# Kernel tuning notes

Hardware: AMD Instinct MI355X
Metric: run time of the kernel (lower is better)

Reference implementation:

```python
import jax, jax.numpy as jnp
import numpy as np

B, N, D, R, STEPS = 16, 512, 512, 8, 2


def setup_inputs() -> dict:
    key = jax.random.key(0)
    ks = jax.random.split(key, 8)
    nodes = jax.random.normal(ks[0], (B, N, D), dtype=jnp.float32)
    edges = jax.random.uniform(ks[1], (B, R, N, N), dtype=jnp.float32)
    scale = 1.0 / np.sqrt(D)
    # per-relation Linear layers: weight [out,in] torch-style, bias [out]
    msg_W = jax.random.uniform(ks[2], (R, D, D), minval=-scale, maxval=scale, dtype=jnp.float32)
    msg_b = jax.random.uniform(ks[3], (R, D), minval=-scale, maxval=scale, dtype=jnp.float32)
    # GRUCell params, gate order (r, z, n) like torch
    w_ih = jax.random.uniform(ks[4], (3 * D, D), minval=-scale, maxval=scale, dtype=jnp.float32)
    w_hh = jax.random.uniform(ks[5], (3 * D, D), minval=-scale, maxval=scale, dtype=jnp.float32)
    b_ih = jax.random.uniform(ks[6], (3 * D,), minval=-scale, maxval=scale, dtype=jnp.float32)
    b_hh = jax.random.uniform(ks[7], (3 * D,), minval=-scale, maxval=scale, dtype=jnp.float32)
    return {"nodes": nodes, "edges": edges, "msg_W": msg_W, "msg_b": msg_b,
            "w_ih": w_ih, "w_hh": w_hh, "b_ih": b_ih, "b_hh": b_hh}


def reference(nodes, edges, msg_W, msg_b, w_ih, w_hh, b_ih, b_hh):
    # nodes: [b,n,d], edges: [b,R,n,n]
    h = nodes  # keep [b,n,d]; torch flattens to [b*n,d] but math is identical
    bias_sum = msg_b.sum(axis=0)  # sum of per-relation biases, [d]
    for _ in range(STEPS):
        # per-relation message passing: m[b,r,i,d] = edges[b,r] @ h[b]
        m = jnp.einsum('brij,bjd->brid', edges, h)
        # per-relation Linear (y = x @ W_r^T + b_r), summed over relations
        agg = jnp.einsum('brid,red->bie', m, msg_W) + bias_sum  # [b,n,d]
        # GRUCell update (gate order r, z, n)
        gi = agg @ w_ih.T + b_ih  # [b,n,3d]
        gh = h @ w_hh.T + b_hh    # [b,n,3d]
        ir, iz, i_n = jnp.split(gi, 3, axis=-1)
        hr, hz, h_n = jnp.split(gh, 3, axis=-1)
        r = jax.nn.sigmoid(ir + hr)
        z = jax.nn.sigmoid(iz + hz)
        n_t = jnp.tanh(i_n + r * h_n)
        h = (1.0 - z) * n_t + z * h
    return h.mean(axis=1)  # [b,d]
```

## Files before the change

### kernel.cpp

```cpp
#include <hip/hip_runtime.h>

typedef _Float16 f16;
typedef __attribute__((ext_vector_type(8))) _Float16 half8;
typedef __attribute__((ext_vector_type(4))) float f32x4;

struct f16x4 { f16 a, b, c, d; };


__device__ __forceinline__ void stage16(const f16* g, f16* l) {
  __builtin_amdgcn_global_load_lds(
      (const __attribute__((address_space(1))) void*)g,
      (__attribute__((address_space(3))) void*)l, 16, 0, 0);
}

__global__ void cvt_fr(const float* __restrict__ in, f16* __restrict__ hi,
                       f16* __restrict__ lo, int n_units) {
  const int u = blockIdx.x * blockDim.x + threadIdx.x;
  if (u >= n_units) return;
  const int l = u & 63, kc = (u >> 6) & 15, rt = u >> 10;
  const long ibase = (long)(rt * 16 + (l & 15)) * 512 + kc * 32 + ((l >> 4) << 3);
  const float4 v0 = *(const float4*)(in + ibase);
  const float4 v1 = *(const float4*)(in + ibase + 4);
  const float v[8] = {v0.x, v0.y, v0.z, v0.w, v1.x, v1.y, v1.z, v1.w};
  half8 h, lw;
#pragma unroll
  for (int e = 0; e < 8; ++e) {
    h[e] = (f16)v[e];
    lw[e] = (f16)(v[e] - (float)h[e]);
  }
  *(half8*)(hi + (long)u * 8) = h;
  *(half8*)(lo + (long)u * 8) = lw;
}

__global__ void cvt_fr1(const float* __restrict__ in, f16* __restrict__ hi,
                        int n_units) {
  const int u = blockIdx.x * blockDim.x + threadIdx.x;
  if (u >= n_units) return;
  const int l = u & 63, kc = (u >> 6) & 15, rt = u >> 10;
  const long ibase = (long)(rt * 16 + (l & 15)) * 512 + kc * 32 + ((l >> 4) << 3);
  const float4 v0 = *(const float4*)(in + ibase);
  const float4 v1 = *(const float4*)(in + ibase + 4);
  const float v[8] = {v0.x, v0.y, v0.z, v0.w, v1.x, v1.y, v1.z, v1.w};
  half8 h;
#pragma unroll
  for (int e = 0; e < 8; ++e) h[e] = (f16)v[e];
  *(half8*)(hi + (long)u * 8) = h;
}

__global__ void bias_sum_k(const float* __restrict__ msg_b, float* __restrict__ bs) {
  int e = threadIdx.x;
  float s = 0.f;
  for (int r = 0; r < 8; ++r) s += msg_b[r * 512 + e];
  bs[e] = s;
}

template <int SA, int SB, int OUT, int SWZ>
__global__ __launch_bounds__(256, 3) void gemm_dr(
    const f16* __restrict__ Ah, const f16* __restrict__ Al,
    const f16* __restrict__ Bh, const f16* __restrict__ Bl,
    f16* __restrict__ Chi, f16* __restrict__ Clo, float* __restrict__ Cf,
    const float* __restrict__ bias, int N, int R, long sAr, long sBr,
    int zdiv, long sAzr, long sAzb, long sBzr, long sBzb,
    long sCzr, long sCzb) {
  constexpr int NU = 8 * ((1 + SA) + (1 + SB));
  constexpr int NW = NU / 4;
  constexpr int BUF = NU * 512;
  constexpr int SMEMN = (2 * BUF > 16384) ? 2 * BUF : 16384;
  __shared__ __align__(16) f16 smem[SMEMN];

  const int tid = threadIdx.x;
  int bx, by, z;
  if constexpr (SWZ) {
    const int l = blockIdx.x;
    const int xcd = l & 7, m2 = l >> 3, zq = m2 >> 4, t = m2 & 15;
    z = (zq << 3) | xcd; bx = t & 3; by = t >> 2;
  } else {
    bx = blockIdx.x; by = blockIdx.y; z = blockIdx.z;
  }
  const int zr = z % zdiv, zb = z / zdiv;
  const int lane = tid & 63;
  const int w = tid >> 6;
  const int wm = (w & 1) << 6;
  const int wn = (w >> 1) << 6;

  const f16* gA = Ah + (long)zr * sAzr + (long)zb * sAzb + (long)by * 65536 + lane * 8;
  const f16* gB = Bh + (long)zr * sBzr + (long)zb * sBzb + (long)bx * 65536 + lane * 8;
  const f16* gAl = SA ? (Al + (gA - Ah)) : nullptr;
  const f16* gBl = SB ? (Bl + (gB - Bh)) : nullptr;
  const long cbase = (long)zr * sCzr + (long)zb * sCzb;

  f32x4 acc[4][4];
#pragma unroll
  for (int i = 0; i < 4; ++i)
#pragma unroll
    for (int j = 0; j < 4; ++j) acc[i][j] = (f32x4){0.f, 0.f, 0.f, 0.f};

  const int NIT = R * 16;

  auto ST = [&](int bf, int ii) {
    const long oa = (long)(ii >> 4) * sAr + (ii & 15) * 512;
    const long ob = (long)(ii >> 4) * sBr + (ii & 15) * 512;
    f16* lb = &smem[bf * BUF];
#pragma unroll
    for (int q = 0; q < NW; ++q) {
      const int s = w * NW + q;
      const f16* src;
      if (s < 8) {
        src = gA + (long)s * 8192 + oa;
      } else if (SA && s < 16) {
        src = gAl + (long)(s - 8) * 8192 + oa;
      } else {
        const int sb = s - 8 * (1 + SA);
        src = (SB && sb >= 8) ? (gBl + (long)(sb - 8) * 8192 + ob)
                              : (gB + (long)sb * 8192 + ob);
      }
      stage16(src, lb + s * 512);
    }
  };

  auto CP = [&](int bf) {
    const f16* lb = &smem[bf * BUF];
    const int lo8 = lane * 8;
    half8 bh[4], bl[4];
#pragma unroll
    for (int nt = 0; nt < 4; ++nt) {
      const int ub = 8 * (1 + SA) + (w >> 1) * 4 + nt;
      bh[nt] = *(const half8*)(lb + ub * 512 + lo8);
      if constexpr (SB) bl[nt] = *(const half8*)(lb + (ub + 8) * 512 + lo8);
    }
#pragma unroll
    for (int mt = 0; mt < 4; ++mt) {
      const int ua = (w & 1) * 4 + mt;
      const half8 ah = *(const half8*)(lb + ua * 512 + lo8);
      half8 al;
      if constexpr (SA) al = *(const half8*)(lb + (ua + 8) * 512 + lo8);
#pragma unroll
      for (int nt = 0; nt < 4; ++nt) {
        acc[mt][nt] = __builtin_amdgcn_mfma_f32_16x16x32_f16(
            ah, bh[nt], acc[mt][nt], 0, 0, 0);
        if constexpr (SB)
          acc[mt][nt] = __builtin_amdgcn_mfma_f32_16x16x32_f16(
              ah, bl[nt], acc[mt][nt], 0, 0, 0);
        if constexpr (SA)
          acc[mt][nt] = __builtin_amdgcn_mfma_f32_16x16x32_f16(
              al, bh[nt], acc[mt][nt], 0, 0, 0);
      }
    }
  };

  auto WAITN = [&]() {
    if constexpr (NW == 4)      asm volatile("s_waitcnt vmcnt(4)" ::: "memory");
    else if constexpr (NW == 6) asm volatile("s_waitcnt vmcnt(6)" ::: "memory");
    else if constexpr (NW == 8) asm volatile("s_waitcnt vmcnt(8)" ::: "memory");
    else                        asm volatile("s_waitcnt vmcnt(0)" ::: "memory");
  };

  ST(0, 0);
  ST(1, 1);
  int cur = 0;
  for (int t = 0; t < NIT; ++t) {
    if (t < NIT - 1) WAITN();
    else asm volatile("s_waitcnt vmcnt(0)" ::: "memory");
    __builtin_amdgcn_s_barrier();
    __builtin_amdgcn_sched_barrier(0);
    CP(cur);
    asm volatile("s_waitcnt lgkmcnt(0)" ::: "memory");
    __builtin_amdgcn_s_barrier();
    if (t + 2 < NIT) ST(cur, t + 2);
    cur ^= 1;
  }
  __syncthreads();

  const int l15 = lane & 15;
  const int rb = (lane >> 4) << 2;
  if constexpr (OUT) {
#pragma unroll
    for (int nt = 0; nt < 4; ++nt) {
      const int col = wn + nt * 16 + l15;
#pragma unroll
      for (int mt = 0; mt < 4; ++mt)
#pragma unroll
        for (int v = 0; v < 4; ++v) {
          const int row = wm + mt * 16 + rb + v;
          const float cval = acc[mt][nt][v];
          const f16 h = (f16)cval;
          smem[row * 128 + ((col >> 3) ^ (row & 15)) * 8 + (col & 7)] = h;
          acc[mt][nt][v] = cval - (float)h;
        }
    }
    __syncthreads();
#pragma unroll
    for (int i2 = 0; i2 < 8; ++i2) {
      const int u = i2 * 256 + tid;
      const int ul = u & 63, kc_loc = (u >> 6) & 3, rt_loc = u >> 8;
      const int row = rt_loc * 16 + (ul & 15);
      const int gcol = kc_loc * 4 + (ul >> 4);
      const int4 vv = *(const int4*)&smem[row * 128 + ((gcol ^ (row & 15)) << 3)];
      *(int4*)&Chi[cbase + ((long)(by * 8 + rt_loc) * 16 + bx * 4 + kc_loc) * 512 + ul * 8] = vv;
    }
    __syncthreads();
#pragma unroll
    for (int nt = 0; nt < 4; ++nt) {
      const int col = wn + nt * 16 + l15;
#pragma unroll
      for (int mt = 0; mt < 4; ++mt)
#pragma unroll
        for (int v = 0; v < 4; ++v) {
          const int row = wm + mt * 16 + rb + v;
          smem[row * 128 + ((col >> 3) ^ (row & 15)) * 8 + (col & 7)] = (f16)acc[mt][nt][v];
        }
    }
    __syncthreads();
#pragma unroll
    for (int i2 = 0; i2 < 8; ++i2) {
      const int u = i2 * 256 + tid;
      const int ul = u & 63, kc_loc = (u >> 6) & 3, rt_loc = u >> 8;
      const int row = rt_loc * 16 + (ul & 15);
      const int gcol = kc_loc * 4 + (ul >> 4);
      const int4 vv = *(const int4*)&smem[row * 128 + ((gcol ^ (row & 15)) << 3)];
      *(int4*)&Clo[cbase + ((long)(by * 8 + rt_loc) * 16 + bx * 4 + kc_loc) * 512 + ul * 8] = vv;
    }
  } else {
#pragma unroll
    for (int nt = 0; nt < 4; ++nt) {
      const int col = bx * 128 + wn + nt * 16 + l15;
      const float bv = bias ? bias[col] : 0.f;
#pragma unroll
      for (int mt = 0; mt < 4; ++mt) {
        const long rowbase = (long)(by * 128 + wm + mt * 16 + rb) * N + col;
#pragma unroll
        for (int v = 0; v < 4; ++v)
          Cf[cbase + rowbase + (long)v * N] = acc[mt][nt][v] + bv;
      }
    }
  }
}

__global__ void reduce_agg2(const f16* __restrict__ Phi, const f16* __restrict__ Plo,
                            const float* __restrict__ bsum,
                            f16* __restrict__ hi, f16* __restrict__ lo) {
  const long i = ((long)blockIdx.x * blockDim.x + threadIdx.x) * 4;
  const int li = (int)i;
  const int l = (li >> 3) & 63, kc = (li >> 9) & 15;
  const int e0 = kc * 32 + ((l >> 4) << 3) + (li & 4);
  const float4 b = *(const float4*)(bsum + e0);
  float v0 = b.x, v1 = b.y, v2 = b.z, v3 = b.w;
#pragma unroll
  for (int q = 0; q < 2; ++q) {
    const long o = (long)q * 4194304 + i;
    const f16x4 ph = *(const f16x4*)(Phi + o);
    const f16x4 pl = *(const f16x4*)(Plo + o);
    v0 += (float)ph.a + (float)pl.a;
    v1 += (float)ph.b + (float)pl.b;
    v2 += (float)ph.c + (float)pl.c;
    v3 += (float)ph.d + (float)pl.d;
  }
  f16x4 h, lw;
  h.a = (f16)v0; lw.a = (f16)(v0 - (float)h.a);
  h.b = (f16)v1; lw.b = (f16)(v1 - (float)h.b);
  h.c = (f16)v2; lw.c = (f16)(v2 - (float)h.c);
  h.d = (f16)v3; lw.d = (f16)(v3 - (float)h.d);
  *(f16x4*)(hi + i) = h;
  *(f16x4*)(lo + i) = lw;
}

__global__ void gru_k(const float* __restrict__ gi, const float* __restrict__ gh,
                      const float* __restrict__ holdf, f16* __restrict__ hhi) {
  const int u = blockIdx.x * blockDim.x + threadIdx.x;
  const int row = u >> 6, d0 = (u & 63) << 3;
  const long gbase = (long)row * 1536 + d0;
  const float4 giR0 = *(const float4*)(gi + gbase),      giR1 = *(const float4*)(gi + gbase + 4);
  const float4 giZ0 = *(const float4*)(gi + gbase + 512), giZ1 = *(const float4*)(gi + gbase + 516);
  const float4 giN0 = *(const float4*)(gi + gbase + 1024), giN1 = *(const float4*)(gi + gbase + 1028);
  const float4 ghR0 = *(const float4*)(gh + gbase),      ghR1 = *(const float4*)(gh + gbase + 4);
  const float4 ghZ0 = *(const float4*)(gh + gbase + 512), ghZ1 = *(const float4*)(gh + gbase + 516);
  const float4 ghN0 = *(const float4*)(gh + gbase + 1024), ghN1 = *(const float4*)(gh + gbase + 1028);
  const float irv[8] = {giR0.x, giR0.y, giR0.z, giR0.w, giR1.x, giR1.y, giR1.z, giR1.w};
  const float izv[8] = {giZ0.x, giZ0.y, giZ0.z, giZ0.w, giZ1.x, giZ1.y, giZ1.z, giZ1.w};
  const float inv[8] = {giN0.x, giN0.y, giN0.z, giN0.w, giN1.x, giN1.y, giN1.z, giN1.w};
  const float hrv[8] = {ghR0.x, ghR0.y, ghR0.z, ghR0.w, ghR1.x, ghR1.y, ghR1.z, ghR1.w};
  const float hzv[8] = {ghZ0.x, ghZ0.y, ghZ0.z, ghZ0.w, ghZ1.x, ghZ1.y, ghZ1.z, ghZ1.w};
  const float hnv[8] = {ghN0.x, ghN0.y, ghN0.z, ghN0.w, ghN1.x, ghN1.y, ghN1.z, ghN1.w};
  const long hflat = (long)(row >> 4) * 8192 + (d0 >> 5) * 512 +
                     ((row & 15) + (((d0 >> 3) & 3) << 4)) * 8;
  half8 hh8;
  if (!holdf) hh8 = *(const half8*)(hhi + hflat);
  half8 oh;
#pragma unroll
  for (int e = 0; e < 8; ++e) {
    const float h = holdf ? holdf[(long)row * 512 + d0 + e] : (float)hh8[e];
    const float r = 1.f / (1.f + __expf(-(irv[e] + hrv[e])));
    const float zg = 1.f / (1.f + __expf(-(izv[e] + hzv[e])));
    const float nt = tanhf(inv[e] + r * hnv[e]);
    const float o = (1.f - zg) * nt + zg * h;
    oh[e] = (f16)o;
  }
  *(half8*)(hhi + hflat) = oh;
}

__global__ void mean_k(const f16* __restrict__ hhi, float* __restrict__ out) {
  const int b = blockIdx.x;
  const int d = threadIdx.x;
  const long base = (long)b * 262144 + (d >> 5) * 512 + (((d >> 3) & 3) << 4) * 8 + (d & 7);
  float s = 0.f;
  for (int n = 0; n < 512; ++n) {
    const long j = base + (long)(n >> 4) * 8192 + (n & 15) * 8;
    s += (float)hhi[j];
  }
  out[b * 512 + d] = s * (1.f / 512.f);
}

extern "C" void kernel_launch(void* const* d_in, const int* in_sizes, int n_in,
                              void* d_out, int out_size, void* d_ws, size_t ws_size,
                              hipStream_t stream) {
  const float* nodes = (const float*)d_in[0];
  const float* edges = (const float*)d_in[1];
  const float* msg_W = (const float*)d_in[2];
  const float* msg_b = (const float*)d_in[3];
  const float* w_ih  = (const float*)d_in[4];
  const float* w_hh  = (const float*)d_in[5];
  const float* b_ih  = (const float*)d_in[6];
  const float* b_hh  = (const float*)d_in[7];
  float* out = (float*)d_out;

  char* ws = (char*)d_ws;
  size_t off = 0;
  auto alloc = [&](size_t bytes) -> char* {
    char* p = ws + off;
    off += (bytes + 1023) & ~(size_t)1023;
    return p;
  };
  f16* edges_hi = (f16*)alloc(33554432ull * 2);
  f16* W_hi     = (f16*)alloc(2097152ull * 2);
  f16* W_lo     = (f16*)alloc(2097152ull * 2);
  f16* wih_hi   = (f16*)alloc(786432ull * 2);
  f16* whh_hi   = (f16*)alloc(786432ull * 2);
  f16* h_hi     = (f16*)alloc(4194304ull * 2);
  f16* hWT_hi   = (f16*)alloc(33554432ull * 2);
  f16* hWT_lo   = (f16*)alloc(33554432ull * 2);
  f16* Phi      = (f16*)alloc(16777216ull * 2);
  f16* Plo      = (f16*)alloc(16777216ull * 2);
  float* bsum   = (float*)alloc(512 * 4);
  float* gi = (float*)hWT_hi;
  float* gh = (float*)hWT_lo;
  f16* agg_hi = hWT_hi + 25165824;
  f16* agg_lo = agg_hi + 4194304;

  cvt_fr1<<<16384, 256, 0, stream>>>(edges, edges_hi, 4194304);
  cvt_fr<<<1024,  256, 0, stream>>>(msg_W, W_hi, W_lo, 262144);
  cvt_fr1<<<384,  256, 0, stream>>>(w_ih, wih_hi, 98304);
  cvt_fr1<<<384,  256, 0, stream>>>(w_hh, whh_hi, 98304);
  cvt_fr1<<<2048, 256, 0, stream>>>(nodes, h_hi, 524288);
  bias_sum_k<<<1, 512, 0, stream>>>(msg_b, bsum);

  for (int step = 0; step < 2; ++step) {
    gemm_dr<1, 0, 1, 0><<<dim3(4, 4, 128), 256, 0, stream>>>(
        W_hi, W_lo, h_hi, nullptr, hWT_hi, hWT_lo, nullptr, nullptr,
        512, 1, 0L, 0L, 8, 262144L, 0L, 0L, 262144L, 262144L, 2097152L);
    gemm_dr<0, 1, 1, 1><<<dim3(512, 1, 1), 256, 0, stream>>>(
        edges_hi, nullptr, hWT_hi, hWT_lo, Phi, Plo, nullptr, nullptr,
        512, 4, 262144L, 262144L, 2, 1048576L, 2097152L, 1048576L, 2097152L,
        4194304L, 262144L);
    reduce_agg2<<<4096, 256, 0, stream>>>(Phi, Plo, bsum, agg_hi, agg_lo);
    gemm_dr<1, 0, 0, 0><<<dim3(12, 64, 1), 256, 0, stream>>>(
        agg_hi, agg_lo, wih_hi, nullptr, nullptr, nullptr, gi, b_ih,
        1536, 1, 0L, 0L, 1, 0L, 0L, 0L, 0L, 0L, 0L);
    gemm_dr<0, 0, 0, 0><<<dim3(12, 64, 1), 256, 0, stream>>>(
        h_hi, nullptr, whh_hi, nullptr, nullptr, nullptr, gh, b_hh,
        1536, 1, 0L, 0L, 1, 0L, 0L, 0L, 0L, 0L, 0L);
    gru_k<<<2048, 256, 0, stream>>>(gi, gh, step ? nullptr : nodes, h_hi);
  }
  mean_k<<<16, 512, 0, stream>>>(h_hi, out);
}
```

Measured before the change: 727.3 us.

## Fuse GRU input/hidden GEMMs into one launch, split mean reduction, merge weight conversions

The two GRU projection GEMMs (agg·W_ih and h·W_hh) now run as a single launch, with block x-index selecting which one a block computes, through a dedicated double-buffered LDS-staged MFMA body. The final mean is split into a two-stage reduction over 256 blocks instead of 16, and the two weight conversions are merged into one launch. gru_k now always reads h from the f16 buffer instead of the fp32 nodes on the first step. That drops some precision on the first step's old-h term, and the new GEMM path hardcodes dimensions.

```diff
diff --git a/kernel.cpp b/kernel.cpp
--- a/kernel.cpp
+++ b/kernel.cpp
@@ -36,6 +36,24 @@
                         int n_units) {
   const int u = blockIdx.x * blockDim.x + threadIdx.x;
   if (u >= n_units) return;
+  const int l = u & 63, kc = (u >> 6) & 15, rt = u >> 10;
+  const long ibase = (long)(rt * 16 + (l & 15)) * 512 + kc * 32 + ((l >> 4) << 3);
+  const float4 v0 = *(const float4*)(in + ibase);
+  const float4 v1 = *(const float4*)(in + ibase + 4);
+  const float v[8] = {v0.x, v0.y, v0.z, v0.w, v1.x, v1.y, v1.z, v1.w};
+  half8 h;
+#pragma unroll
+  for (int e = 0; e < 8; ++e) h[e] = (f16)v[e];
+  *(half8*)(hi + (long)u * 8) = h;
+}
+
+__global__ void cvt_fr1_2(const float* __restrict__ inA, f16* __restrict__ hiA,
+                          const float* __restrict__ inB, f16* __restrict__ hiB,
+                          int nA) {
+  int u = blockIdx.x * blockDim.x + threadIdx.x;
+  const float* in = inA;
+  f16* hi = hiA;
+  if (u >= nA) { u -= nA; in = inB; hi = hiB; }
   const int l = u & 63, kc = (u >> 6) & 15, rt = u >> 10;
   const long ibase = (long)(rt * 16 + (l & 15)) * 512 + kc * 32 + ((l >> 4) << 3);
   const float4 v0 = *(const float4*)(in + ibase);
@@ -236,6 +254,112 @@
   }
 }
 
+template <int SA>
+__device__ __forceinline__ void gemm_body(
+    const f16* __restrict__ Ah, const f16* __restrict__ Al,
+    const f16* __restrict__ Bh, float* __restrict__ Cf,
+    const float* __restrict__ bias, int bx, int by, f16* smem) {
+  constexpr int NU = 8 * (1 + SA) + 8;
+  constexpr int NW = NU / 4;
+  constexpr int BUF = NU * 512;
+
+  const int tid = threadIdx.x;
+  const int lane = tid & 63;
+  const int w = tid >> 6;
+  const int wm = (w & 1) << 6;
+  const int wn = (w >> 1) << 6;
+
+  const f16* gA = Ah + (long)by * 65536 + lane * 8;
+  const f16* gB = Bh + (long)bx * 65536 + lane * 8;
+  const f16* gAl = SA ? (Al + (gA - Ah)) : nullptr;
+
+  f32x4 acc[4][4];
+#pragma unroll
+  for (int i = 0; i < 4; ++i)
+#pragma unroll
+    for (int j = 0; j < 4; ++j) acc[i][j] = (f32x4){0.f, 0.f, 0.f, 0.f};
+
+  auto ST = [&](int bf, int ii) {
+    const long oa = (long)ii * 512;
+    f16* lb = &smem[bf * BUF];
+#pragma unroll
+    for (int q = 0; q < NW; ++q) {
+      const int s = w * NW + q;
+      const f16* src;
+      if (s < 8) src = gA + (long)s * 8192 + oa;
+      else if (SA && s < 16) src = gAl + (long)(s - 8) * 8192 + oa;
+      else src = gB + (long)(s - 8 * (1 + SA)) * 8192 + oa;
+      stage16(src, lb + s * 512);
+    }
+  };
+  auto CP = [&](int bf) {
+    const f16* lb = &smem[bf * BUF];
+    const int lo8 = lane * 8;
+    half8 bh[4];
+#pragma unroll
+    for (int nt = 0; nt < 4; ++nt)
+      bh[nt] = *(const half8*)(lb + (8 * (1 + SA) + (w >> 1) * 4 + nt) * 512 + lo8);
+#pragma unroll
+    for (int mt = 0; mt < 4; ++mt) {
+      const int ua = (w & 1) * 4 + mt;
+      const half8 ah = *(const half8*)(lb + ua * 512 + lo8);
+      half8 al;
+      if constexpr (SA) al = *(const half8*)(lb + (ua + 8) * 512 + lo8);
+#pragma unroll
+      for (int nt = 0; nt < 4; ++nt) {
+        acc[mt][nt] = __builtin_amdgcn_mfma_f32_16x16x32_f16(ah, bh[nt], acc[mt][nt], 0, 0, 0);
+        if constexpr (SA)
+          acc[mt][nt] = __builtin_amdgcn_mfma_f32_16x16x32_f16(al, bh[nt], acc[mt][nt], 0, 0, 0);
+      }
+    }
+  };
+  auto WAITN = [&]() {
+    if constexpr (NW == 4) asm volatile("s_waitcnt vmcnt(4)" ::: "memory");
+    else                   asm volatile("s_waitcnt vmcnt(6)" ::: "memory");
+  };
+
+  ST(0, 0);
+  ST(1, 1);
+  int cur = 0;
+  for (int t = 0; t < 16; ++t) {
+    if (t < 15) WAITN();
+    else asm volatile("s_waitcnt vmcnt(0)" ::: "memory");
+    __builtin_amdgcn_s_barrier();
+    __builtin_amdgcn_sched_barrier(0);
+    CP(cur);
+    asm volatile("s_waitcnt lgkmcnt(0)" ::: "memory");
+    __builtin_amdgcn_s_barrier();
+    if (t + 2 < 16) ST(cur, t + 2);
+    cur ^= 1;
+  }
+
+  const int l15 = lane & 15;
+  const int rb = (lane >> 4) << 2;
+#pragma unroll
+  for (int nt = 0; nt < 4; ++nt) {
+    const int col = bx * 128 + wn + nt * 16 + l15;
+    const float bv = bias[col];
+#pragma unroll
+    for (int mt = 0; mt < 4; ++mt) {
+      const long rowbase = (long)(by * 128 + wm + mt * 16 + rb) * 1536 + col;
+#pragma unroll
+      for (int v = 0; v < 4; ++v)
+        Cf[rowbase + (long)v * 1536] = acc[mt][nt][v] + bv;
+    }
+  }
+}
+
+__global__ __launch_bounds__(256, 3) void gemm_34(
+    const f16* __restrict__ agg_hi, const f16* __restrict__ agg_lo,
+    const f16* __restrict__ wih, const f16* __restrict__ h_hi,
+    const f16* __restrict__ whh, float* __restrict__ gi, float* __restrict__ gh,
+    const float* __restrict__ b_ih, const float* __restrict__ b_hh) {
+  __shared__ __align__(16) f16 smem[24576];
+  const int bx = blockIdx.x, by = blockIdx.y;
+  if (bx < 12) gemm_body<1>(agg_hi, agg_lo, wih, gi, b_ih, bx, by, smem);
+  else         gemm_body<0>(h_hi, nullptr, whh, gh, b_hh, bx - 12, by, smem);
+}
+
 __global__ void reduce_agg2(const f16* __restrict__ Phi, const f16* __restrict__ Plo,
                             const float* __restrict__ bsum,
                             f16* __restrict__ hi, f16* __restrict__ lo) {
@@ -265,7 +389,7 @@
 }
 
 __global__ void gru_k(const float* __restrict__ gi, const float* __restrict__ gh,
-                      const float* __restrict__ holdf, f16* __restrict__ hhi) {
+                      f16* __restrict__ hhi) {
   const int u = blockIdx.x * blockDim.x + threadIdx.x;
   const int row = u >> 6, d0 = (u & 63) << 3;
   const long gbase = (long)row * 1536 + d0;
@@ -283,12 +407,11 @@
   const float hnv[8] = {ghN0.x, ghN0.y, ghN0.z, ghN0.w, ghN1.x, ghN1.y, ghN1.z, ghN1.w};
   const long hflat = (long)(row >> 4) * 8192 + (d0 >> 5) * 512 +
                      ((row & 15) + (((d0 >> 3) & 3) << 4)) * 8;
-  half8 hh8;
-  if (!holdf) hh8 = *(const half8*)(hhi + hflat);
+  const half8 hh8 = *(const half8*)(hhi + hflat);
   half8 oh;
 #pragma unroll
   for (int e = 0; e < 8; ++e) {
-    const float h = holdf ? holdf[(long)row * 512 + d0 + e] : (float)hh8[e];
+    const float h = (float)hh8[e];
     const float r = 1.f / (1.f + __expf(-(irv[e] + hrv[e])));
     const float zg = 1.f / (1.f + __expf(-(izv[e] + hzv[e])));
     const float nt = tanhf(inv[e] + r * hnv[e]);
@@ -298,15 +421,23 @@
   *(half8*)(hhi + hflat) = oh;
 }
 
-__global__ void mean_k(const f16* __restrict__ hhi, float* __restrict__ out) {
-  const int b = blockIdx.x;
+__global__ void mean1(const f16* __restrict__ hhi, float* __restrict__ part) {
+  const int b = blockIdx.x >> 4, g = blockIdx.x & 15;
   const int d = threadIdx.x;
   const long base = (long)b * 262144 + (d >> 5) * 512 + (((d >> 3) & 3) << 4) * 8 + (d & 7);
   float s = 0.f;
-  for (int n = 0; n < 512; ++n) {
+  for (int n = g * 32; n < g * 32 + 32; ++n) {
     const long j = base + (long)(n >> 4) * 8192 + (n & 15) * 8;
     s += (float)hhi[j];
   }
+  part[(long)blockIdx.x * 512 + d] = s;
+}
+__global__ void mean2(const float* __restrict__ part, float* __restrict__ out) {
+  const int b = blockIdx.x;
+  const int d = threadIdx.x;
+  float s = 0.f;
+#pragma unroll
+  for (int g = 0; g < 16; ++g) s += part[(long)(b * 16 + g) * 512 + d];
   out[b * 512 + d] = s * (1.f / 512.f);
 }
 
@@ -341,6 +472,7 @@
   f16* Phi      = (f16*)alloc(16777216ull * 2);
   f16* Plo      = (f16*)alloc(16777216ull * 2);
   float* bsum   = (float*)alloc(512 * 4);
+  float* mpart  = (float*)alloc(131072ull * 4);
   float* gi = (float*)hWT_hi;
   float* gh = (float*)hWT_lo;
   f16* agg_hi = hWT_hi + 25165824;
@@ -348,8 +480,7 @@
 
   cvt_fr1<<<16384, 256, 0, stream>>>(edges, edges_hi, 4194304);
   cvt_fr<<<1024,  256, 0, stream>>>(msg_W, W_hi, W_lo, 262144);
-  cvt_fr1<<<384,  256, 0, stream>>>(w_ih, wih_hi, 98304);
-  cvt_fr1<<<384,  256, 0, stream>>>(w_hh, whh_hi, 98304);
+  cvt_fr1_2<<<768, 256, 0, stream>>>(w_ih, wih_hi, w_hh, whh_hi, 98304);
   cvt_fr1<<<2048, 256, 0, stream>>>(nodes, h_hi, 524288);
   bias_sum_k<<<1, 512, 0, stream>>>(msg_b, bsum);
 
@@ -362,13 +493,10 @@
         512, 4, 262144L, 262144L, 2, 1048576L, 2097152L, 1048576L, 2097152L,
         4194304L, 262144L);
     reduce_agg2<<<4096, 256, 0, stream>>>(Phi, Plo, bsum, agg_hi, agg_lo);
-    gemm_dr<1, 0, 0, 0><<<dim3(12, 64, 1), 256, 0, stream>>>(
-        agg_hi, agg_lo, wih_hi, nullptr, nullptr, nullptr, gi, b_ih,
-        1536, 1, 0L, 0L, 1, 0L, 0L, 0L, 0L, 0L, 0L);
-    gemm_dr<0, 0, 0, 0><<<dim3(12, 64, 1), 256, 0, stream>>>(
-        h_hi, nullptr, whh_hi, nullptr, nullptr, nullptr, gh, b_hh,
-        1536, 1, 0L, 0L, 1, 0L, 0L, 0L, 0L, 0L, 0L);
-    gru_k<<<2048, 256, 0, stream>>>(gi, gh, step ? nullptr : nodes, h_hi);
-  }
-  mean_k<<<16, 512, 0, stream>>>(h_hi, out);
-}
+    gemm_34<<<dim3(24, 64), 256, 0, stream>>>(
+        agg_hi, agg_lo, wih_hi, h_hi, whh_hi, gi, gh, b_ih, b_hh);
+    gru_k<<<2048, 256, 0, stream>>>(gi, gh, h_hi);
+  }
+  mean1<<<256, 512, 0, stream>>>(h_hi, mpart);
+  mean2<<<16, 512, 0, stream>>>(mpart, out);
+}
```

Measured after the change: 691.8 us, median of 2. 4.9% less time.
